# Kernel tuning notes

Measured on AMD Instinct MI355X. Metric: run time of the kernel, lower is better.

## Reference

```python
import jax, jax.numpy as jnp
import numpy as np

G = 4   # DCNv3 default groups
K = 3   # DCNv3 kernel size
P = K * K


def layernorm(x, g, b, eps=1e-5):
    m = jnp.mean(x, axis=-1, keepdims=True)
    v = jnp.var(x, axis=-1, keepdims=True)
    return (x - m) * jax.lax.rsqrt(v + eps) * g + b


def setup_inputs():
    key = jax.random.key(0)
    ks = jax.random.split(key, 12)
    B, Cin, C, H, W = 2, 64, 64, 512, 512
    s = lambda k, shape, sc=1.0: jax.random.normal(k, shape, jnp.float32) * sc
    return {
        "x": s(ks[0], (B, Cin, H, W)),
        "conv_w": s(ks[1], (C, Cin, 3, 3), 0.05),
        "w_in": s(ks[2], (C, C), 0.1), "b_in": s(ks[3], (C,), 0.1),
        "dw_w": s(ks[4], (3, 3, 1, C), 0.1), "dw_b": s(ks[5], (C,), 0.1),
        "ln_g": jnp.ones((C,), jnp.float32), "ln_b": jnp.zeros((C,), jnp.float32),
        "w_off": s(ks[6], (C, G * P * 2), 0.02), "b_off": s(ks[7], (G * P * 2,), 0.02),
        "w_mask": s(ks[8], (C, G * P), 0.1), "b_mask": s(ks[9], (G * P,), 0.1),
        "w_out": s(ks[10], (C, C), 0.1), "b_out": s(ks[11], (C,), 0.1),
    }


def dcnv3_core(x, offset, mask):
    # x: (N,H,W,C) projected input; offset: (N,H,W,G*P*2); mask: (N,H,W,G,P) softmaxed
    N, H, W, C = x.shape
    gc = C // G
    pad = 1
    xp = jnp.pad(x, ((0, 0), (pad, pad), (pad, pad), (0, 0)))
    Hin, Win = H + 2 * pad, W + 2 * pad
    dt = x.dtype
    # reference points: centers of each 3x3 window on the padded input, normalized
    ref_x = (jnp.arange(W, dtype=dt) + 1.5) / Win  # (dil*(k-1))//2 + 0.5 = 1.5
    ref_y = (jnp.arange(H, dtype=dt) + 1.5) / Hin
    # dilation grid: kx outer, ky inner (matches torch meshgrid 'ij' ordering)
    lin = jnp.arange(K, dtype=dt) - (K - 1) // 2
    gx, gy = jnp.meshgrid(lin, lin, indexing='ij')
    grid = jnp.stack([gx / Win, gy / Hin], -1).reshape(P, 2)  # identical for all groups
    off = offset.reshape(N, H, W, G, P, 2) / jnp.array([Win, Hin], dt)  # offset_scale=1
    loc_x = ref_x[None, None, :, None, None] + grid[:, 0] + off[..., 0]  # (N,H,W,G,P)
    loc_y = ref_y[None, :, None, None, None] + grid[:, 1] + off[..., 1]
    # grid_sample(align_corners=False): pixel = loc*size - 0.5, zero padding outside
    ix = loc_x * Win - 0.5
    iy = loc_y * Hin - 0.5
    x0f = jnp.floor(ix); y0f = jnp.floor(iy)
    fx = ix - x0f; fy = iy - y0f
    x0 = x0f.astype(jnp.int32); y0 = y0f.astype(jnp.int32)
    xg = xp.reshape(N, Hin * Win, G, gc)
    n_idx = jnp.arange(N)[:, None, None, None, None]
    g_idx = jnp.arange(G)[None, None, None, :, None]

    def corner(yc, xc, cw):
        valid = (yc >= 0) & (yc < Hin) & (xc >= 0) & (xc < Win)
        idx = jnp.clip(yc, 0, Hin - 1) * Win + jnp.clip(xc, 0, Win - 1)
        v = xg[n_idx, idx, g_idx]                     # (N,H,W,G,P,gc) irregular gather
        w = cw * valid.astype(dt) * mask              # fold mask into bilinear weight
        return jnp.einsum('nhwgpc,nhwgp->nhwgc', v, w)

    out = (corner(y0, x0, (1 - fy) * (1 - fx))
           + corner(y0, x0 + 1, (1 - fy) * fx)
           + corner(y0 + 1, x0, fy * (1 - fx))
           + corner(y0 + 1, x0 + 1, fy * fx))
    return out.reshape(N, H, W, C)


def reference(x, conv_w, w_in, b_in, dw_w, dw_b, ln_g, ln_b, w_off, b_off, w_mask, b_mask, w_out, b_out):
    # stride-2 'down' conv (no bias), then channels-last ReLU
    y = jax.lax.conv_general_dilated(x, conv_w, (2, 2), ((1, 1), (1, 1)),
                                     dimension_numbers=('NCHW', 'OIHW', 'NCHW'))
    y = jax.nn.relu(jnp.transpose(y, (0, 2, 3, 1)))  # (N,H,W,C)
    N, H, W, C = y.shape
    x_proj = y @ w_in + b_in                         # DCNv3 input_proj
    # depthwise 3x3 conv + LayerNorm + GELU for the offset/mask branch
    x1 = jax.lax.conv_general_dilated(y, dw_w, (1, 1), ((1, 1), (1, 1)),
                                      dimension_numbers=('NHWC', 'HWIO', 'NHWC'),
                                      feature_group_count=C) + dw_b
    x1 = jax.nn.gelu(layernorm(x1, ln_g, ln_b), approximate=False)
    offset = x1 @ w_off + b_off
    m = jax.nn.softmax((x1 @ w_mask + b_mask).reshape(N, H, W, G, P), axis=-1)
    out = dcnv3_core(x_proj, offset, m) @ w_out + b_out  # output_proj
    return jnp.transpose(out, (0, 3, 1, 2))  # back to NCHW
```

## Files before the change

kernel.cpp:

```cpp
#include <hip/hip_runtime.h>
#include <hip/hip_bf16.h>
#include <math.h>

#define NB 2
#define C 64
#define H 256
#define W 256
#define HIN 512
#define WIN 512
#define CIN 64
#define G 4
#define P 9
#define GC 16
#define NPIX (NB*H*W)

typedef __attribute__((ext_vector_type(8))) __bf16 bf16x8v;
typedef __attribute__((ext_vector_type(4))) float floatx4;

#define O_WOUT   47872
#define O_BIN    51968
#define O_DWW    52032
#define O_DWB    52608
#define O_LNG    52672
#define O_LNB    52736
#define O_BOFF   52800
#define O_BMASK  52872
#define O_BOUT   52908
#define O_WFRAG  53248
#define O_WINF   71680
#define O_WCOMB  73728
#define O_Y      77824
#define O_XP     (O_Y  + 8388608)
#define O_OFFS   (O_XP + 8388608)
#define O_MASK   (O_OFFS + 9437184)

static __device__ __forceinline__ unsigned pkbf(float a, float b) {
    unsigned lo = __bfloat16_as_ushort(__float2bfloat16(a));
    unsigned hi = __bfloat16_as_ushort(__float2bfloat16(b));
    return lo | (hi << 16);
}

__global__ void k_prep(const float* __restrict__ conv_w, const float* __restrict__ w_in,
                       const float* __restrict__ b_in,
                       const float* __restrict__ dw_w, const float* __restrict__ dw_b,
                       const float* __restrict__ ln_g, const float* __restrict__ ln_b,
                       const float* __restrict__ w_off, const float* __restrict__ b_off,
                       const float* __restrict__ w_mask, const float* __restrict__ b_mask,
                       const float* __restrict__ w_out, const float* __restrict__ b_out,
                       float* __restrict__ ws)
{
    int i = blockIdx.x*256 + threadIdx.x;
    if (i < 36864) {
        int j    = i & 7;
        int lane = (i >> 3) & 63;
        int nt   = (i >> 9) & 3;
        int ks   = (i >> 11) & 1;
        int tap  = i >> 12;
        int kh = tap / 3, kw = tap % 3;
        int ci = ks*32 + (lane >> 4)*8 + j;
        int co = nt*16 + (lane & 15);
        ((__hip_bfloat16*)(ws + O_WFRAG))[i] =
            __float2bfloat16(conv_w[co*576 + ci*9 + kh*3 + kw]);
    }
    if (i < 4096) {
        int j    = i & 7;
        int lane = (i >> 3) & 63;
        int s    = i >> 9;
        int nt   = s & 3, ks = s >> 2;
        int ci = ks*32 + (lane >> 4)*8 + j;
        int co = nt*16 + (lane & 15);
        ((__hip_bfloat16*)(ws + O_WINF))[i] = __float2bfloat16(w_in[ci*64 + co]);
    }
    if (i < 7168) {
        int j    = i & 7;
        int lane = (i >> 3) & 63;
        int s    = i >> 9;
        int nt   = s % 7, ks = s / 7;
        int ci = ks*32 + (lane >> 4)*8 + j;
        int jj = nt*16 + (lane & 15);
        float v = (jj < 72) ? w_off[ci*72 + jj] : (jj < 108 ? w_mask[ci*36 + (jj-72)] : 0.f);
        ((__hip_bfloat16*)(ws + O_WCOMB))[i] = __float2bfloat16(v);
    }
    if (i < 4096) ws[O_WOUT + i] = w_out[i];
    if (i < 64)   ws[O_BIN  + i] = b_in[i];
    if (i < 576)  ws[O_DWW  + i] = dw_w[i];
    if (i < 64)   ws[O_DWB  + i] = dw_b[i];
    if (i < 64)   ws[O_LNG  + i] = ln_g[i];
    if (i < 64)   ws[O_LNB  + i] = ln_b[i];
    if (i < 72)   ws[O_BOFF + i] = b_off[i];
    if (i < 36)   ws[O_BMASK+ i] = b_mask[i];
    if (i < 64)   ws[O_BOUT + i] = b_out[i];
}

__global__ __launch_bounds__(256) void k_xt(
    const float* __restrict__ x, __hip_bfloat16* __restrict__ xt)
{
    __shared__ float tile[64][65];
    int t = threadIdx.x;
    int b = blockIdx.x;
    int n  = b >> 12;
    int p0 = (b & 4095) * 64;
    const float* xb = x + (size_t)n*CIN*262144;
    #pragma unroll
    for (int k=0;k<16;k++) {
        int ch = k*4 + (t>>6);
        int px = t & 63;
        tile[px][ch] = xb[(size_t)ch*262144 + p0 + px];
    }
    __syncthreads();
    #pragma unroll
    for (int k=0;k<2;k++) {
        int e = k*256 + t;
        int px = e >> 3;
        int c8 = (e & 7)*8;
        __hip_bfloat16 v[8];
        #pragma unroll
        for (int j=0;j<8;j++) v[j] = __float2bfloat16(tile[px][c8+j]);
        *(uint4*)(xt + ((size_t)(n*262144 + p0 + px))*64 + c8) = *(uint4*)v;
    }
}

__global__ __launch_bounds__(256) void k_conv_mfma(
    const __hip_bfloat16* __restrict__ xt, const float* __restrict__ ws,
    float* __restrict__ y)
{
    const __hip_bfloat16* wf = (const __hip_bfloat16*)(ws + O_WFRAG);
    int t = threadIdx.x, lane = t & 63, wv = t >> 6;
    int pix0 = blockIdx.x*64 + wv*16;
    int n = pix0 >> 16;
    int hw = pix0 & 65535;
    int h = hw >> 8, wo0 = hw & 255;
    int m = lane & 15, q = lane >> 4;
    floatx4 acc[4] = {};
    #pragma unroll
    for (int kh=0; kh<3; kh++) {
        int ih = 2*h + kh - 1;
        if (ih < 0) continue;
        size_t rowbase = ((size_t)(n*512 + ih))*512;
        #pragma unroll
        for (int kw=0; kw<3; kw++) {
            int iw = 2*wo0 + kw - 1 + 2*m;
            bool inval = iw < 0;
            int iwc = inval ? 0 : iw;
            const __hip_bfloat16* ap = xt + (rowbase + iwc)*64 + q*8;
            const __hip_bfloat16* bp = wf + (kh*3 + kw)*4096 + lane*8;
            #pragma unroll
            for (int ks=0; ks<2; ks++) {
                uint4 au = *(const uint4*)(ap + ks*32);
                if (inval) au = make_uint4(0,0,0,0);
                bf16x8v av = __builtin_bit_cast(bf16x8v, au);
                #pragma unroll
                for (int nt=0; nt<4; nt++) {
                    uint4 bu = *(const uint4*)(bp + ks*2048 + nt*512);
                    bf16x8v bv = __builtin_bit_cast(bf16x8v, bu);
                    acc[nt] = __builtin_amdgcn_mfma_f32_16x16x32_bf16(av, bv, acc[nt], 0,0,0);
                }
            }
        }
    }
    int co0 = lane & 15;
    #pragma unroll
    for (int nt=0; nt<4; nt++)
        #pragma unroll
        for (int r=0; r<4; r++)
            y[((size_t)(pix0 + q*4 + r))*64 + nt*16 + co0] = fmaxf(acc[nt][r], 0.f);
}

__global__ __launch_bounds__(256) void k_branch(
    const float* __restrict__ y, const float* __restrict__ ws,
    float* __restrict__ offs, float* __restrict__ mask, float* __restrict__ xp)
{
    __shared__ float scr[64][68];
    __shared__ __align__(16) __hip_bfloat16 x1b[64][72];
    __shared__ __align__(16) __hip_bfloat16 ysb[64][72];
    int t = threadIdx.x;
    int lane = t & 63;
    int wv = t >> 6;
    int pix0 = blockIdx.x * 64;
    int n  = pix0 >> 16;
    int hw = pix0 & 65535;
    int hh = hw >> 8, ww0 = hw & 255;
    float dwv[9];
    #pragma unroll
    for (int k=0;k<9;k++) dwv[k] = ws[O_DWW + k*C + lane];
    float dbb = ws[O_DWB + lane];
    const float* ybase = y + (size_t)(n*H)*W*C + lane;
    #pragma unroll
    for (int rg=0; rg<4; rg++) {
        int i0 = wv*16 + rg*4;
        int cb = ww0 + i0 - 1;
        float cc[3][6];
        #pragma unroll
        for (int kh=0; kh<3; kh++) {
            int yh = hh + kh - 1;
            bool rv = (yh >= 0) && (yh < H);
            const float* yr = ybase + (size_t)(rv ? yh : 0)*W*C;
            #pragma unroll
            for (int c=0; c<6; c++) {
                int col = cb + c;
                bool ok = rv && (col >= 0) && (col < W);
                cc[kh][c] = ok ? yr[(ptrdiff_t)col*C] : 0.f;
            }
        }
        float a[4];
        #pragma unroll
        for (int u=0; u<4; u++) a[u] = dbb;
        #pragma unroll
        for (int kh=0; kh<3; kh++)
            #pragma unroll
            for (int kw=0; kw<3; kw++) {
                float wg = dwv[kh*3+kw];
                #pragma unroll
                for (int u=0; u<4; u++) a[u] = fmaf(cc[kh][u+kw], wg, a[u]);
            }
        #pragma unroll
        for (int u=0; u<4; u++) {
            scr[i0+u][lane] = a[u];
            ysb[i0+u][lane] = __float2bfloat16(cc[1][u+1]);
        }
    }
    asm volatile("" ::: "memory");
    {
        int pxl = lane >> 2;
        int cq  = lane & 3;
        int i   = wv*16 + pxl;
        const float* ar = &scr[i][cq*16];
        float4 V0 = *(const float4*)(ar);
        float4 V1 = *(const float4*)(ar + 4);
        float4 V2 = *(const float4*)(ar + 8);
        float4 V3 = *(const float4*)(ar + 12);
        float v[16] = {V0.x,V0.y,V0.z,V0.w, V1.x,V1.y,V1.z,V1.w,
                       V2.x,V2.y,V2.z,V2.w, V3.x,V3.y,V3.z,V3.w};
        float s = 0.f, s2 = 0.f;
        #pragma unroll
        for (int k=0;k<16;k++) { s += v[k]; s2 = fmaf(v[k], v[k], s2); }
        s  += __shfl_xor(s,  1, 64);  s  += __shfl_xor(s,  2, 64);
        s2 += __shfl_xor(s2, 1, 64);  s2 += __shfl_xor(s2, 2, 64);
        float mean = s * 0.015625f;
        float var  = fmaxf(fmaf(-mean, mean, s2 * 0.015625f), 0.f);
        float rsig = rsqrtf(var + 1e-5f);
        const float* gp = ws + O_LNG + cq*16;
        const float* bp = ws + O_LNB + cq*16;
        float4 Ga = *(const float4*)gp,      Gb = *(const float4*)(gp+4);
        float4 Gc = *(const float4*)(gp+8),  Gd = *(const float4*)(gp+12);
        float4 Ba = *(const float4*)bp,      Bb = *(const float4*)(bp+4);
        float4 Bc = *(const float4*)(bp+8),  Bd = *(const float4*)(bp+12);
        float gv[16] = {Ga.x,Ga.y,Ga.z,Ga.w, Gb.x,Gb.y,Gb.z,Gb.w,
                        Gc.x,Gc.y,Gc.z,Gc.w, Gd.x,Gd.y,Gd.z,Gd.w};
        float bv[16] = {Ba.x,Ba.y,Ba.z,Ba.w, Bb.x,Bb.y,Bb.z,Bb.w,
                        Bc.x,Bc.y,Bc.z,Bc.w, Bd.x,Bd.y,Bd.z,Bd.w};
        float gl[16];
        #pragma unroll
        for (int k=0;k<16;k++) {
            float xh = fmaf((v[k]-mean)*rsig, gv[k], bv[k]);
            gl[k] = 0.5f * xh * (1.f + erff(xh * 0.70710678118654752f));
        }
        uint4 w0, w1;
        w0.x = pkbf(gl[0],gl[1]);  w0.y = pkbf(gl[2],gl[3]);
        w0.z = pkbf(gl[4],gl[5]);  w0.w = pkbf(gl[6],gl[7]);
        w1.x = pkbf(gl[8],gl[9]);  w1.y = pkbf(gl[10],gl[11]);
        w1.z = pkbf(gl[12],gl[13]);w1.w = pkbf(gl[14],gl[15]);
        *(uint4*)&x1b[i][cq*16]     = w0;
        *(uint4*)&x1b[i][cq*16 + 8] = w1;
    }
    asm volatile("" ::: "memory");
    int m = lane & 15, q = lane >> 4;
    bf16x8v af[2];
    #pragma unroll
    for (int ks=0; ks<2; ks++)
        af[ks] = __builtin_bit_cast(bf16x8v, *(const uint4*)&x1b[wv*16 + m][ks*32 + q*8]);
    const __hip_bfloat16* wcomb = (const __hip_bfloat16*)(ws + O_WCOMB);
    #pragma unroll
    for (int nt=0; nt<7; nt++) {
        int j = nt*16 + m;
        float b = (j < 72) ? ws[O_BOFF + j] : (j < 108 ? ws[O_BMASK + j - 72] : 0.f);
        floatx4 acc = {b,b,b,b};
        #pragma unroll
        for (int ks=0; ks<2; ks++) {
            uint4 bu = *(const uint4*)(wcomb + (ks*7 + nt)*512 + lane*8);
            bf16x8v bvv = __builtin_bit_cast(bf16x8v, bu);
            acc = __builtin_amdgcn_mfma_f32_16x16x32_bf16(af[ks], bvv, acc, 0,0,0);
        }
        if (j < 72) {
            #pragma unroll
            for (int r=0;r<4;r++)
                offs[(size_t)(pix0 + wv*16 + q*4 + r)*72 + j] = acc[r];
        } else if (j < 108) {
            int jj = j - 72;
            int gg = jj / 9, qq = jj - gg*9;
            #pragma unroll
            for (int r=0;r<4;r++)
                scr[wv*16 + q*4 + r][gg*12 + qq] = acc[r];
        }
    }
    {
        const __hip_bfloat16* wfin = (const __hip_bfloat16*)(ws + O_WINF);
        bf16x8v af2[2];
        #pragma unroll
        for (int ks=0; ks<2; ks++) {
            uint4 u = *(const uint4*)&ysb[wv*16 + m][ks*32 + q*8];
            af2[ks] = __builtin_bit_cast(bf16x8v, u);
        }
        #pragma unroll
        for (int nt=0; nt<4; nt++) {
            float b = ws[O_BIN + nt*16 + m];
            floatx4 a2 = {b,b,b,b};
            #pragma unroll
            for (int ks=0; ks<2; ks++) {
                uint4 bu = *(const uint4*)(wfin + (ks*4 + nt)*512 + lane*8);
                bf16x8v bvv = __builtin_bit_cast(bf16x8v, bu);
                a2 = __builtin_amdgcn_mfma_f32_16x16x32_bf16(af2[ks], bvv, a2, 0,0,0);
            }
            #pragma unroll
            for (int r=0;r<4;r++)
                xp[((size_t)(pix0 + wv*16 + q*4 + r))*64 + nt*16 + m] = a2[r];
        }
    }
    asm volatile("" ::: "memory");
    {
        int pxl = lane >> 2;
        int i   = wv*16 + pxl;
        int g   = lane & 3;
        const float* lrow = &scr[i][g*12];
        float l[9];
        #pragma unroll
        for (int qq=0;qq<9;qq++) l[qq] = lrow[qq];
        float mx = l[0];
        #pragma unroll
        for (int qq=1;qq<9;qq++) mx = fmaxf(mx, l[qq]);
        float e[9]; float sum = 0.f;
        #pragma unroll
        for (int qq=0;qq<9;qq++) { e[qq] = expf(l[qq]-mx); sum += e[qq]; }
        float rs = 1.f / sum;
        float* mp = mask + (size_t)(pix0 + i)*36 + g*9;
        #pragma unroll
        for (int qq=0;qq<9;qq++) mp[qq] = e[qq] * rs;
    }
}

#define DPX 16
__global__ __launch_bounds__(256, 4) void k_dcn(
    const float* __restrict__ xp, const float* __restrict__ offs,
    const float* __restrict__ mask, const float* __restrict__ ws,
    float* __restrict__ out)
{
    __shared__ float core[DPX][68];
    __shared__ float ot[64][17];
    __shared__ __align__(16) float offsl[DPX*72];
    __shared__ __align__(16) float maskl[DPX*36];
    __shared__ __align__(16) float wsl[4096];
    int t = threadIdx.x;
    int lane = t & 63;
    int wv = t >> 6;
    int bid = blockIdx.x;
    int nbk = (bid & 7) * (gridDim.x >> 3) + (bid >> 3);
    int pix0 = nbk * DPX;
    {
        const float4* osrc = (const float4*)(offs + (size_t)pix0*72);
        float4* odst = (float4*)offsl;
        odst[t] = osrc[t];
        if (t < 32) odst[256 + t] = osrc[256 + t];
        const float4* msrc = (const float4*)(mask + (size_t)pix0*36);
        float4* mdst = (float4*)maskl;
        if (t < 144) mdst[t] = msrc[t];
        const float4* wsrc = (const float4*)(ws + O_WOUT);
        float4* wdst = (float4*)wsl;
        #pragma unroll
        for (int k=0;k<4;k++) wdst[k*256 + t] = wsrc[k*256 + t];
    }
    __syncthreads();
    int c4  = lane & 3;
    int g   = (lane >> 2) & 3;
    int sub = lane >> 4;
    int i   = wv*4 + sub;
    int pix = pix0 + i;
    int n  = pix >> 16;
    int hw = pix & 65535;
    int hh = hw >> 8, ww = hw & 255;
    const float* ob  = offsl + i*72 + g*18;
    const float* mb  = maskl + i*36 + g*9;
    const float* xpb = xp + (size_t)n*H*W*C + g*GC + c4*4;
    int   eo[P][4];
    float wv4[P][4];
    #pragma unroll
    for (int p=0;p<P;p++) {
        const int kx = p/3, ky = p%3;
        float offx = ob[p*2], offy = ob[p*2+1];
        float mm = mb[p];
        float ix = (float)(ww + kx) + offx;
        float iy = (float)(hh + ky) + offy;
        float x0f = floorf(ix), y0f = floorf(iy);
        float fx = ix - x0f, fy = iy - y0f;
        int x0 = (int)x0f - 1, y0 = (int)y0f - 1;
        int x1 = x0 + 1,       y1 = y0 + 1;
        bool vx0 = (x0 >= 0) & (x0 < W), vx1 = (x1 >= 0) & (x1 < W);
        bool vy0 = (y0 >= 0) & (y0 < H), vy1 = (y1 >= 0) & (y1 < H);
        int cx0 = min(max(x0,0), W-1), cx1 = min(max(x1,0), W-1);
        int ry0 = min(max(y0,0), H-1) * W, ry1 = min(max(y1,0), H-1) * W;
        float am = (1.f - fy) * mm, bm = fy * mm;
        float fxc = 1.f - fx;
        eo[p][0] = (ry0 + cx0) * C;  wv4[p][0] = (vy0 & vx0) ? am * fxc : 0.f;
        eo[p][1] = (ry0 + cx1) * C;  wv4[p][1] = (vy0 & vx1) ? am * fx  : 0.f;
        eo[p][2] = (ry1 + cx0) * C;  wv4[p][2] = (vy1 & vx0) ? bm * fxc : 0.f;
        eo[p][3] = (ry1 + cx1) * C;  wv4[p][3] = (vy1 & vx1) ? bm * fx  : 0.f;
    }
    floatx4 ac0 = {0.f,0.f,0.f,0.f}, ac1 = {0.f,0.f,0.f,0.f};
    #pragma unroll
    for (int p=0;p<P;p++) {
        float4 v0 = *(const float4*)(xpb + eo[p][0]);
        float4 v1 = *(const float4*)(xpb + eo[p][1]);
        float4 v2 = *(const float4*)(xpb + eo[p][2]);
        float4 v3 = *(const float4*)(xpb + eo[p][3]);
        float w0 = wv4[p][0], w1 = wv4[p][1], w2 = wv4[p][2], w3 = wv4[p][3];
        ac0[0] = fmaf(v0.x, w0, fmaf(v1.x, w1, ac0[0]));
        ac0[1] = fmaf(v0.y, w0, fmaf(v1.y, w1, ac0[1]));
        ac0[2] = fmaf(v0.z, w0, fmaf(v1.z, w1, ac0[2]));
        ac0[3] = fmaf(v0.w, w0, fmaf(v1.w, w1, ac0[3]));
        ac1[0] = fmaf(v2.x, w2, fmaf(v3.x, w3, ac1[0]));
        ac1[1] = fmaf(v2.y, w2, fmaf(v3.y, w3, ac1[1]));
        ac1[2] = fmaf(v2.z, w2, fmaf(v3.z, w3, ac1[2]));
        ac1[3] = fmaf(v2.w, w2, fmaf(v3.w, w3, ac1[3]));
    }
    float4 acc;
    acc.x = ac0[0] + ac1[0];
    acc.y = ac0[1] + ac1[1];
    acc.z = ac0[2] + ac1[2];
    acc.w = ac0[3] + ac1[3];
    *(float4*)&core[i][g*GC + c4*4] = acc;
    __syncthreads();
    {
        int cq = t & 15, px = t >> 4;
        float4 a = *(const float4*)(ws + O_BOUT + cq*4);
        #pragma unroll 4
        for (int c=0;c<64;c+=4) {
            float4 cv = *(const float4*)&core[px][c];
            const float* wp = wsl + c*64 + cq*4;
            float4 w0 = *(const float4*)(wp);
            float4 w1 = *(const float4*)(wp + 64);
            float4 w2 = *(const float4*)(wp + 128);
            float4 w3 = *(const float4*)(wp + 192);
            a.x += cv.x*w0.x + cv.y*w1.x + cv.z*w2.x + cv.w*w3.x;
            a.y += cv.x*w0.y + cv.y*w1.y + cv.z*w2.y + cv.w*w3.y;
            a.z += cv.x*w0.z + cv.y*w1.z + cv.z*w2.z + cv.w*w3.z;
            a.w += cv.x*w0.w + cv.y*w1.w + cv.z*w2.w + cv.w*w3.w;
        }
        ot[cq*4+0][px] = a.x;
        ot[cq*4+1][px] = a.y;
        ot[cq*4+2][px] = a.z;
        ot[cq*4+3][px] = a.w;
    }
    __syncthreads();
    {
        int n2 = pix0 >> 16, hw0 = pix0 & 65535;
        float* ob2 = out + (size_t)n2*C*65536 + hw0;
        #pragma unroll
        for (int k=0;k<4;k++) {
            int e = k*256 + t;
            int co = e >> 4, ppx = e & 15;
            ob2[(size_t)co*65536 + ppx] = ot[co][ppx];
        }
    }
}

extern "C" void kernel_launch(void* const* d_in, const int* in_sizes, int n_in,
                              void* d_out, int out_size, void* d_ws, size_t ws_size,
                              hipStream_t stream)
{
    const float* x     = (const float*)d_in[0];
    const float* convw = (const float*)d_in[1];
    const float* w_in  = (const float*)d_in[2];
    const float* b_in  = (const float*)d_in[3];
    const float* dw_w  = (const float*)d_in[4];
    const float* dw_b  = (const float*)d_in[5];
    const float* ln_g  = (const float*)d_in[6];
    const float* ln_b  = (const float*)d_in[7];
    const float* w_off = (const float*)d_in[8];
    const float* b_off = (const float*)d_in[9];
    const float* w_mask= (const float*)d_in[10];
    const float* b_mask= (const float*)d_in[11];
    const float* w_out = (const float*)d_in[12];
    const float* b_out = (const float*)d_in[13];

    float* ws   = (float*)d_ws;
    float* y    = ws + O_Y;
    float* xp   = ws + O_XP;
    float* offs = ws + O_OFFS;
    float* mask = ws + O_MASK;
    __hip_bfloat16* xt = (__hip_bfloat16*)(ws + O_XP);

    k_prep<<<144, 256, 0, stream>>>(convw, w_in, b_in, dw_w, dw_b, ln_g, ln_b,
                                    w_off, b_off, w_mask, b_mask, w_out, b_out, ws);
    k_xt<<<8192, 256, 0, stream>>>(x, xt);
    k_conv_mfma<<<2048, 256, 0, stream>>>(xt, ws, y);
    k_branch<<<NPIX/64, 256, 0, stream>>>(y, ws, offs, mask, xp);
    k_dcn<<<NPIX/DPX, 256, 0, stream>>>(xp, offs, mask, ws, (float*)d_out);
}
```

Baseline: 362.5 us.

## Fuse NCHW-to-bf16 transpose into stride-2 conv via swizzled LDS tile

Removes the separate transpose kernel that wrote a channels-last bf16 copy of the input. The conv kernel now loads the three needed fp32 input rows directly, converts them to bf16 and stores them in an XOR-swizzled shared-memory tile that the MFMA loop reads. This avoids writing and rereading the intermediate tensor. In exchange, input rows shared between neighbouring output rows are fetched from global memory more than once, and the kernel uses about 50KB of LDS, which may limit occupancy.

Result: slower. 444.4 us (+22.6%).

```diff
diff --git a/kernel.cpp b/kernel.cpp
--- a/kernel.cpp
+++ b/kernel.cpp
@@ -92,62 +92,63 @@
     if (i < 64)   ws[O_BOUT + i] = b_out[i];
 }
 
-__global__ __launch_bounds__(256) void k_xt(
-    const float* __restrict__ x, __hip_bfloat16* __restrict__ xt)
-{
-    __shared__ float tile[64][65];
-    int t = threadIdx.x;
-    int b = blockIdx.x;
-    int n  = b >> 12;
-    int p0 = (b & 4095) * 64;
-    const float* xb = x + (size_t)n*CIN*262144;
-    #pragma unroll
-    for (int k=0;k<16;k++) {
-        int ch = k*4 + (t>>6);
-        int px = t & 63;
-        tile[px][ch] = xb[(size_t)ch*262144 + p0 + px];
-    }
-    __syncthreads();
-    #pragma unroll
-    for (int k=0;k<2;k++) {
-        int e = k*256 + t;
-        int px = e >> 3;
-        int c8 = (e & 7)*8;
-        __hip_bfloat16 v[8];
-        #pragma unroll
-        for (int j=0;j<8;j++) v[j] = __float2bfloat16(tile[px][c8+j]);
-        *(uint4*)(xt + ((size_t)(n*262144 + p0 + px))*64 + c8) = *(uint4*)v;
-    }
-}
-
+#define CROWB 16896
 __global__ __launch_bounds__(256) void k_conv_mfma(
-    const __hip_bfloat16* __restrict__ xt, const float* __restrict__ ws,
+    const float* __restrict__ x, const float* __restrict__ ws,
     float* __restrict__ y)
 {
+    __shared__ __align__(16) unsigned char xtile[3*CROWB];
     const __hip_bfloat16* wf = (const __hip_bfloat16*)(ws + O_WFRAG);
     int t = threadIdx.x, lane = t & 63, wv = t >> 6;
-    int pix0 = blockIdx.x*64 + wv*16;
-    int n = pix0 >> 16;
-    int hw = pix0 & 65535;
-    int h = hw >> 8, wo0 = hw & 255;
+    int bid = blockIdx.x;
+    int pix0 = bid*64 + wv*16;
+    int n   = bid >> 10;
+    int h   = (bid >> 2) & 255;
+    int wo0 = (bid & 3) * 64;
+    int cb  = 2*wo0 - 1;
+    const float* xb = x + (size_t)n*CIN*262144;
+    #pragma unroll
+    for (int k=0;k<12;k++) {
+        int u   = k*4 + wv;
+        int row = u >> 4;
+        int oct = (u >> 1) & 7;
+        int seg = u & 1;
+        int col = seg*64 + lane;
+        int gcol = cb + col;
+        int ih  = 2*h - 1 + row;
+        bool ok = (gcol >= 0) && (ih >= 0);
+        const float* src = xb + (size_t)(oct*8)*262144
+                              + (size_t)(ok ? ih : 0)*512 + (ok ? gcol : 0);
+        float v[8];
+        #pragma unroll
+        for (int j=0;j<8;j++) v[j] = ok ? src[(size_t)j*262144] : 0.f;
+        uint4 pk;
+        pk.x = pkbf(v[0],v[1]); pk.y = pkbf(v[2],v[3]);
+        pk.z = pkbf(v[4],v[5]); pk.w = pkbf(v[6],v[7]);
+        int chunk = oct ^ (col & 7);
+        *(uint4*)(xtile + row*CROWB + col*128 + chunk*16) = pk;
+    }
+    if (t < 192) {
+        int row = t >> 6, ch = t & 63;
+        int ih = 2*h - 1 + row;
+        int gcol = cb + 128;
+        float v = (ih >= 0) ? xb[(size_t)ch*262144 + (size_t)ih*512 + gcol] : 0.f;
+        *(__hip_bfloat16*)(xtile + row*CROWB + 128*128 + (ch>>3)*16 + (ch&7)*2) =
+            __float2bfloat16(v);
+    }
+    __syncthreads();
     int m = lane & 15, q = lane >> 4;
     floatx4 acc[4] = {};
     #pragma unroll
     for (int kh=0; kh<3; kh++) {
-        int ih = 2*h + kh - 1;
-        if (ih < 0) continue;
-        size_t rowbase = ((size_t)(n*512 + ih))*512;
         #pragma unroll
         for (int kw=0; kw<3; kw++) {
-            int iw = 2*wo0 + kw - 1 + 2*m;
-            bool inval = iw < 0;
-            int iwc = inval ? 0 : iw;
-            const __hip_bfloat16* ap = xt + (rowbase + iwc)*64 + q*8;
+            int col = 2*(wv*16 + m) + kw;
             const __hip_bfloat16* bp = wf + (kh*3 + kw)*4096 + lane*8;
             #pragma unroll
             for (int ks=0; ks<2; ks++) {
-                uint4 au = *(const uint4*)(ap + ks*32);
-                if (inval) au = make_uint4(0,0,0,0);
+                uint4 au = *(const uint4*)(xtile + kh*CROWB + col*128
+                                           + (((q + ks*4) ^ (col & 7))*16));
                 bf16x8v av = __builtin_bit_cast(bf16x8v, au);
                 #pragma unroll
                 for (int nt=0; nt<4; nt++) {
@@ -486,12 +487,10 @@
     float* xp   = ws + O_XP;
     float* offs = ws + O_OFFS;
     float* mask = ws + O_MASK;
-    __hip_bfloat16* xt = (__hip_bfloat16*)(ws + O_XP);
 
     k_prep<<<144, 256, 0, stream>>>(convw, w_in, b_in, dw_w, dw_b, ln_g, ln_b,
                                     w_off, b_off, w_mask, b_mask, w_out, b_out, ws);
-    k_xt<<<8192, 256, 0, stream>>>(x, xt);
-    k_conv_mfma<<<2048, 256, 0, stream>>>(xt, ws, y);
+    k_conv_mfma<<<2048, 256, 0, stream>>>(x, ws, y);
     k_branch<<<NPIX/64, 256, 0, stream>>>(y, ws, offs, mask, xp);
     k_dcn<<<NPIX/DPX, 256, 0, stream>>>(xp, offs, mask, ws, (float*)d_out);
 }
```
